# Performance work log

Measured on AMD Instinct MI355X. Metric: run time of the kernel, lower is better.

Reference implementation:

```python
import jax, jax.numpy as jnp
import numpy as np

E = 512; H = 512; L = 3; NH = 8; HD = H // NH; V = 32000
B = 64; S = 64; T = 20


def setup_inputs() -> dict:
    key = jax.random.key(0)
    ks = jax.random.split(key, 14)
    sc = 0.02
    return {
        "encoder_out": jax.random.normal(ks[0], (B, S, H), jnp.float32),
        "captions": jax.random.randint(ks[1], (B, T), 0, V),
        "embed_table": jax.random.normal(ks[2], (V, E), jnp.float32) * sc,
        "w_ih": jax.random.normal(ks[3], (L, 3 * H, E), jnp.float32) * sc,
        "w_hh": jax.random.normal(ks[4], (L, 3 * H, H), jnp.float32) * sc,
        "b_ih": jax.random.normal(ks[5], (L, 3 * H), jnp.float32) * sc,
        "b_hh": jax.random.normal(ks[6], (L, 3 * H), jnp.float32) * sc,
        "in_proj_w": jax.random.normal(ks[7], (3 * H, H), jnp.float32) * sc,
        "in_proj_b": jax.random.normal(ks[8], (3 * H,), jnp.float32) * sc,
        "out_proj_w": jax.random.normal(ks[9], (H, H), jnp.float32) * sc,
        "out_proj_b": jax.random.normal(ks[10], (H,), jnp.float32) * sc,
        "fc_w": jax.random.normal(ks[11], (V, H), jnp.float32) * sc,
        "fc_b": jax.random.normal(ks[12], (V,), jnp.float32) * sc,
    }


def _gru_cell(x, h, Wih, Whh, bih, bhh):
    # PyTorch GRUCell math. x: (B, in), h: (B, H)
    gi = x @ Wih.T + bih  # (B, 3H)
    gh = h @ Whh.T + bhh
    i_r, i_z, i_n = jnp.split(gi, 3, axis=-1)
    h_r, h_z, h_n = jnp.split(gh, 3, axis=-1)
    r = jax.nn.sigmoid(i_r + h_r)
    z = jax.nn.sigmoid(i_z + h_z)
    n = jnp.tanh(i_n + r * h_n)
    return (1.0 - z) * n + z * h


def reference(encoder_out, captions, embed_table, w_ih, w_hh, b_ih, b_hh,
              in_proj_w, in_proj_b, out_proj_w, out_proj_b, fc_w, fc_b):
    Wq, Wk, Wv = jnp.split(in_proj_w, 3, axis=0)
    bq, bk, bv = jnp.split(in_proj_b, 3, axis=0)
    # K/V projections of encoder_out are timestep-invariant: precompute once.
    Kh = (encoder_out @ Wk.T + bk).reshape(B, S, NH, HD)
    Vh = (encoder_out @ Wv.T + bv).reshape(B, S, NH, HD)
    scale = 1.0 / jnp.sqrt(jnp.float32(HD))

    emb = embed_table[captions]              # (B, T, E)
    xs = jnp.transpose(emb, (1, 0, 2))       # (T, B, E)

    def step(h, x_t):
        # h: (L, B, H); x_t: (B, E)
        new_h = []
        inp = x_t
        for l in range(L):
            hl = _gru_cell(inp, h[l], w_ih[l], w_hh[l], b_ih[l], b_hh[l])
            new_h.append(hl)
            inp = hl
        q = (inp @ Wq.T + bq).reshape(B, NH, HD)
        scores = jnp.einsum('bnd,bsnd->bns', q, Kh) * scale
        attn = jax.nn.softmax(scores, axis=-1)
        ctx = jnp.einsum('bns,bsnd->bnd', attn, Vh).reshape(B, H)
        ao = ctx @ out_proj_w.T + out_proj_b
        logits = ao @ fc_w.T + fc_b           # (B, V)
        return jnp.stack(new_h), logits

    h0 = jnp.zeros((L, B, H), dtype=encoder_out.dtype)
    _, logits = jax.lax.scan(step, h0, xs)    # logits: (T, B, V)
    return jnp.transpose(logits, (1, 0, 2))   # (B, T, V)
```

## Files before the change

kernel.cpp:

```cpp
#include <hip/hip_runtime.h>
#include <hip/hip_bf16.h>

#define TT 20
#define BB 64
#define HH 512
#define EE 512
#define VV 32000
#define NBLK 32

typedef __bf16 bf16x8 __attribute__((ext_vector_type(8)));
typedef float f32x4 __attribute__((ext_vector_type(4)));
typedef unsigned long long u64;

template <int L> struct IC { static constexpr int value = L; };

__device__ __forceinline__ void gload_lds16(const __hip_bfloat16* g, __hip_bfloat16* l) {
    __builtin_amdgcn_global_load_lds((const __attribute__((address_space(1))) void*)g,
                                     (__attribute__((address_space(3))) void*)l, 16, 0, 0);
}

__device__ __forceinline__ float sigmf(float x) { return 1.f / (1.f + __expf(-x)); }

__device__ __forceinline__ void cstore8B(void* p, u64 v) {
    __hip_atomic_store((u64*)p, v, __ATOMIC_RELAXED, __HIP_MEMORY_SCOPE_AGENT);
}
__device__ __forceinline__ void cstore4B(void* p, unsigned v) {
    __hip_atomic_store((unsigned*)p, v, __ATOMIC_RELAXED, __HIP_MEMORY_SCOPE_AGENT);
}


__global__ __launch_bounds__(256) void f2bf_kernel(const float* __restrict__ in,
                                                   __hip_bfloat16* __restrict__ out, int n) {
    int i = blockIdx.x * 256 + threadIdx.x;
    if (i < n) out[i] = __float2bfloat16(in[i]);
}

__global__ __launch_bounds__(256) void gather_emb_kernel(const float* __restrict__ tab,
                                                         const int* __restrict__ cap,
                                                         __hip_bfloat16* __restrict__ out) {
    int i = blockIdx.x * 256 + threadIdx.x;
    int e = i & (EE - 1);
    int tb = i >> 9;
    int t = tb >> 6;
    int b = tb & 63;
    int tok = cap[b * TT + t];
    out[i] = __float2bfloat16(tab[(size_t)tok * EE + e]);
}

__global__ __launch_bounds__(256) void init_kernel(__hip_bfloat16* __restrict__ hbuf,
                                                   int* __restrict__ bar) {
    int i = blockIdx.x * 256 + threadIdx.x;
    hbuf[i] = __float2bfloat16(0.f);
    if (i < 64) bar[i] = 0;
}


__global__ __launch_bounds__(256) void gemm128_kernel(
    const __hip_bfloat16* __restrict__ A,
    const __hip_bfloat16* __restrict__ Bm,
    const float* __restrict__ bias,
    float* __restrict__ C,
    __hip_bfloat16* __restrict__ Cb,
    int K, int N)
{
    __shared__ __align__(16) __hip_bfloat16 As[128 * 32];
    __shared__ __align__(16) __hip_bfloat16 Bs[128 * 32];

    int m0 = blockIdx.x * 128, n0 = blockIdx.y * 128;
    int tid = threadIdx.x;
    int wave = tid >> 6, lane = tid & 63;
    int wm = wave & 1, wn = wave >> 1;
    int row16 = lane & 15, quad = lane >> 4;

    int r0 = tid >> 2, cc = (tid & 3) * 8;
    int r1 = 64 + r0;
    const __hip_bfloat16* gA0 = A  + (size_t)(m0 + r0) * K + cc;
    const __hip_bfloat16* gA1 = A  + (size_t)(m0 + r1) * K + cc;
    const __hip_bfloat16* gB0 = Bm + (size_t)(n0 + r0) * K + cc;
    const __hip_bfloat16* gB1 = Bm + (size_t)(n0 + r1) * K + cc;
    __hip_bfloat16* lA0 = As + (size_t)(wave * 64) * 8;
    __hip_bfloat16* lA1 = As + (size_t)(256 + wave * 64) * 8;
    __hip_bfloat16* lB0 = Bs + (size_t)(wave * 64) * 8;
    __hip_bfloat16* lB1 = Bs + (size_t)(256 + wave * 64) * 8;

    const __hip_bfloat16* ra = As + (size_t)(wm * 64 + row16) * 32 + quad * 8;
    const __hip_bfloat16* rb = Bs + (size_t)(wn * 64 + row16) * 32 + quad * 8;

    f32x4 acc[4][4] = {};

    for (int k = 0; k < K; k += 32) {
        gload_lds16(gA0 + k, lA0);
        gload_lds16(gA1 + k, lA1);
        gload_lds16(gB0 + k, lB0);
        gload_lds16(gB1 + k, lB1);
        __syncthreads();
        bf16x8 af[4], bfr[4];
#pragma unroll
        for (int mt = 0; mt < 4; ++mt)
            af[mt] = *reinterpret_cast<const bf16x8*>(ra + mt * 16 * 32);
#pragma unroll
        for (int nt = 0; nt < 4; ++nt)
            bfr[nt] = *reinterpret_cast<const bf16x8*>(rb + nt * 16 * 32);
#pragma unroll
        for (int mt = 0; mt < 4; ++mt)
#pragma unroll
            for (int nt = 0; nt < 4; ++nt)
                acc[mt][nt] = __builtin_amdgcn_mfma_f32_16x16x32_bf16(af[mt], bfr[nt], acc[mt][nt], 0, 0, 0);
        __syncthreads();
    }

#pragma unroll
    for (int mt = 0; mt < 4; ++mt)
#pragma unroll
        for (int nt = 0; nt < 4; ++nt) {
            int col = n0 + wn * 64 + nt * 16 + row16;
            float bv = bias ? bias[col] : 0.f;
#pragma unroll
            for (int r = 0; r < 4; ++r) {
                int row = m0 + wm * 64 + mt * 16 + quad * 4 + r;
                size_t off = (size_t)row * N + col;
                float v = acc[mt][nt][r] + bv;
                if (Cb) Cb[off] = __float2bfloat16(v);
                else    C[off]  = v;
            }
        }
}


__global__ __launch_bounds__(512) void recurrence_kernel(
    const float* __restrict__ GI0,
    const __hip_bfloat16* __restrict__ wih,
    const __hip_bfloat16* __restrict__ whh,
    const float* __restrict__ bih,
    const float* __restrict__ bhh,
    const __hip_bfloat16* __restrict__ wq,
    const float* __restrict__ bq,
    const __hip_bfloat16* __restrict__ wo,
    const float* __restrict__ bo,
    const __hip_bfloat16* __restrict__ KVb,
    __hip_bfloat16* __restrict__ hbuf,
    float* __restrict__ qrot,
    __hip_bfloat16* __restrict__ ctxrot,
    __hip_bfloat16* __restrict__ AO,
    int* __restrict__ bar)
{
    __shared__ float smem[24 * 544];

    {
        int d = __hip_atomic_load(&bar[1], __ATOMIC_ACQUIRE, __HIP_MEMORY_SCOPE_AGENT);
        asm volatile("" :: "v"(d));
    }
    __syncthreads();

    const int tid = threadIdx.x;
    const int w = tid >> 6, lane = tid & 63;
    const int row16 = lane & 15, quad = lane >> 4;
    const int blk = blockIdx.x;
    const int c0 = blk * 16;
    const size_t HS = (size_t)64 * 512;

    f32x4 h0r = {0.f, 0.f, 0.f, 0.f}, h1r = h0r, h2r = h0r;

    int lgen = 0;
    auto gridbar = [&]() {
        asm volatile("s_waitcnt vmcnt(0)" ::: "memory");
        __syncthreads();
        if (tid == 0) {
            lgen++;
            __hip_atomic_fetch_add(&bar[0], 1, __ATOMIC_RELAXED, __HIP_MEMORY_SCOPE_AGENT);
            while (__hip_atomic_load(&bar[0], __ATOMIC_RELAXED, __HIP_MEMORY_SCOPE_AGENT) < NBLK * lgen)
                __builtin_amdgcn_s_sleep(1);
        }
        __syncthreads();
    };

#define PART(s, r, c) smem[(s) * 544 + (r) * 17 + (c)]

    auto gru_stage = [&](auto LC, int t) {
        constexpr int l = decltype(LC)::value;
        const __hip_bfloat16* hown = hbuf + ((size_t)t * 3 + l) * HS;
        const __hip_bfloat16* xin  = l ? hbuf + ((size_t)(t + 1) * 3 + (l - 1)) * HS : hown;
        const __hip_bfloat16* Wihl = wih + (size_t)l * 1536 * 512;
        const __hip_bfloat16* Whhl = whh + (size_t)l * 1536 * 512;

        int src, rh, kseg, koff;
        constexpr int nk = l ? 8 : 4;
        if (l) { src = w >> 2; rh = (w >> 1) & 1; kseg = w & 1; koff = kseg * 256; }
        else   { src = 1;      rh = w >> 2;       kseg = w & 3; koff = kseg * 128; }

        const __hip_bfloat16* Asrc = src ? hown : xin;
        const __hip_bfloat16* pa = Asrc + (size_t)(rh * 32 + row16) * 512 + koff + quad * 8;
        bf16x8 af0[nk], af1[nk];
#pragma unroll
        for (int kk = 0; kk < nk; ++kk) {
            af0[kk] = *reinterpret_cast<const bf16x8*>(pa + kk * 32);
            af1[kk] = *reinterpret_cast<const bf16x8*>(pa + (size_t)16 * 512 + kk * 32);
        }

        const __hip_bfloat16* pw = (src ? Whhl : Wihl) + (size_t)(c0 + row16) * 512 + koff + quad * 8;
        f32x4 acc[3][2] = {};
#pragma unroll
        for (int kk = 0; kk < nk; ++kk) {
            int kb = kk * 32;
#pragma unroll
            for (int g = 0; g < 3; ++g) {
                bf16x8 wv = *reinterpret_cast<const bf16x8*>(pw + (size_t)g * 262144 + kb);
                acc[g][0] = __builtin_amdgcn_mfma_f32_16x16x32_bf16(af0[kk], wv, acc[g][0], 0, 0, 0);
                acc[g][1] = __builtin_amdgcn_mfma_f32_16x16x32_bf16(af1[kk], wv, acc[g][1], 0, 0, 0);
            }
        }
#pragma unroll
        for (int g = 0; g < 3; ++g) {
            int slot = l ? (g * 8 + src * 4 + rh * 2 + kseg) : (g * 8 + rh * 4 + kseg);
#pragma unroll
            for (int mf = 0; mf < 2; ++mf)
#pragma unroll
                for (int r = 0; r < 4; ++r)
                    PART(slot, mf * 16 + quad * 4 + r, row16) = (mf ? acc[g][1][r] : acc[g][0][r]);
        }
        __syncthreads();

        if (tid < 256) {
            int row = tid >> 2, cg = tid & 3;
            int rh2 = row >> 5, lr = row & 31;
            const float* bihl = bih + l * 1536;
            const float* bhhl = bhh + l * 1536;
            f32x4& hr = (l == 0) ? h0r : (l == 1) ? h1r : h2r;
            f32x4 gi4[3];
            if (!l) {
                const float* gp = GI0 + (size_t)(t * 64 + row) * 1536 + c0 + cg * 4;
#pragma unroll
                for (int g = 0; g < 3; ++g)
                    gi4[g] = *reinterpret_cast<const f32x4*>(gp + g * 512);
            }
            union { unsigned short us[4]; u64 u; } pk;
#pragma unroll
            for (int cc = 0; cc < 4; ++cc) {
                int col16 = cg * 4 + cc, col = c0 + col16;
                float gi[3], gh[3];
#pragma unroll
                for (int g = 0; g < 3; ++g) {
                    if (l) {
                        gi[g] = PART(g * 8 + rh2 * 2, lr, col16) + PART(g * 8 + rh2 * 2 + 1, lr, col16);
                        gh[g] = PART(g * 8 + 4 + rh2 * 2, lr, col16) + PART(g * 8 + 4 + rh2 * 2 + 1, lr, col16);
                    } else {
                        gh[g] = PART(g * 8 + rh2 * 4, lr, col16) + PART(g * 8 + rh2 * 4 + 1, lr, col16) +
                                PART(g * 8 + rh2 * 4 + 2, lr, col16) + PART(g * 8 + rh2 * 4 + 3, lr, col16);
                        gi[g] = gi4[g][cc];
                    }
                }
                float rr = sigmf(gi[0] + gh[0] + bihl[col] + bhhl[col]);
                float zz = sigmf(gi[1] + gh[1] + bihl[512 + col] + bhhl[512 + col]);
                float nn = tanhf(gi[2] + bihl[1024 + col] + rr * (gh[2] + bhhl[1024 + col]));
                float hnew = (1.f - zz) * nn + zz * hr[cc];
                hr[cc] = hnew;
                __hip_bfloat16 hv = __float2bfloat16(hnew);
                pk.us[cc] = *reinterpret_cast<unsigned short*>(&hv);
            }
            cstore8B(hbuf + ((size_t)(t + 1) * 3 + l) * HS + (size_t)row * 512 + c0 + cg * 4, pk.u);
        }
        __syncthreads();
    };

    auto proj_stage = [&](const __hip_bfloat16* Asrc, const __hip_bfloat16* Wm,
                          const float* bias, bool to_q, int t) {
        int rh = w >> 2, kseg = w & 3, koff = kseg * 128;
        const __hip_bfloat16* pa = Asrc + (size_t)(rh * 32 + row16) * 512 + koff + quad * 8;
        bf16x8 af0[4], af1[4];
#pragma unroll
        for (int kk = 0; kk < 4; ++kk) {
            af0[kk] = *reinterpret_cast<const bf16x8*>(pa + kk * 32);
            af1[kk] = *reinterpret_cast<const bf16x8*>(pa + (size_t)16 * 512 + kk * 32);
        }
        const __hip_bfloat16* pw = Wm + (size_t)(c0 + row16) * 512 + koff + quad * 8;
        f32x4 a0 = {0.f, 0.f, 0.f, 0.f}, a1 = a0;
#pragma unroll
        for (int kk = 0; kk < 4; ++kk) {
            bf16x8 wv = *reinterpret_cast<const bf16x8*>(pw + kk * 32);
            a0 = __builtin_amdgcn_mfma_f32_16x16x32_bf16(af0[kk], wv, a0, 0, 0, 0);
            a1 = __builtin_amdgcn_mfma_f32_16x16x32_bf16(af1[kk], wv, a1, 0, 0, 0);
        }
#pragma unroll
        for (int r = 0; r < 4; ++r) {
            PART(w, quad * 4 + r, row16) = a0[r];
            PART(w, 16 + quad * 4 + r, row16) = a1[r];
        }
        __syncthreads();
        if (tid < 256) {
            int row = tid >> 2, cg = tid & 3;
            int rh2 = row >> 5, lr = row & 31;
            float v[4];
#pragma unroll
            for (int cc = 0; cc < 4; ++cc) {
                int col16 = cg * 4 + cc;
                float s = bias[c0 + col16];
#pragma unroll
                for (int ks = 0; ks < 4; ++ks) s += PART(rh2 * 4 + ks, lr, col16);
                v[cc] = s;
            }
            if (to_q) {
                float* dst = qrot + (size_t)t * HS + (size_t)row * 512 + c0 + cg * 4;
                union { float f[2]; u64 u; } p0, p1;
                p0.f[0] = v[0]; p0.f[1] = v[1];
                p1.f[0] = v[2]; p1.f[1] = v[3];
                cstore8B(dst, p0.u);
                cstore8B(dst + 2, p1.u);
            } else {
                union { unsigned short us[4]; u64 u; } pk;
#pragma unroll
                for (int cc = 0; cc < 4; ++cc) {
                    __hip_bfloat16 hv = __float2bfloat16(v[cc]);
                    pk.us[cc] = *reinterpret_cast<unsigned short*>(&hv);
                }
                cstore8B(AO + ((size_t)row * TT + t) * 512 + c0 + cg * 4, pk.u);
            }
        }
        __syncthreads();
    };

    auto attn_stage = [&](int t) {
        float* qls = smem;
        const float* qsrc = qrot + (size_t)t * HS;
        if (tid < 256) {
            int rr = tid >> 7, off = (tid & 127) * 4;
            f32x4 v = *reinterpret_cast<const f32x4*>(qsrc + (size_t)(blk + rr * 32) * 512 + off);
            *reinterpret_cast<f32x4*>(qls + rr * 512 + off) = v;
        }
        __syncthreads();
#pragma unroll 1
        for (int rr = 0; rr < 2; ++rr) {
            int b = blk + rr * 32;
            const float* qh = qls + rr * 512 + w * 64;
            const __hip_bfloat16* kr = KVb + (size_t)(b * 64 + lane) * 1024 + w * 64;
            float sc = 0.f;
#pragma unroll
            for (int k8 = 0; k8 < 8; ++k8) {
                bf16x8 kv = *reinterpret_cast<const bf16x8*>(kr + k8 * 8);
                const float* qv = qh + k8 * 8;
#pragma unroll
                for (int e = 0; e < 8; ++e) sc += qv[e] * (float)kv[e];
            }
            sc *= 0.125f;
            float m = sc;
            for (int off = 32; off; off >>= 1) m = fmaxf(m, __shfl_xor(m, off, 64));
            float e = __expf(sc - m);
            float s = e;
            for (int off = 32; off; off >>= 1) s += __shfl_xor(s, off, 64);
            float p = e / s;
            const __hip_bfloat16* vb = KVb + (size_t)(b * 64) * 1024 + 512 + w * 64 + lane;
            float acc = 0.f;
#pragma unroll
            for (int si = 0; si < 64; ++si)
                acc += __shfl(p, si, 64) * (float)vb[(size_t)si * 1024];
            float hi = __shfl_down(acc, 1, 64);
            if (!(lane & 1)) {
                __hip_bfloat16 e0 = __float2bfloat16(acc), e1 = __float2bfloat16(hi);
                unsigned pk = (unsigned)*reinterpret_cast<unsigned short*>(&e0) |
                              ((unsigned)*reinterpret_cast<unsigned short*>(&e1) << 16);
                cstore4B(ctxrot + (size_t)t * HS + (size_t)b * 512 + w * 64 + lane, pk);
            }
        }
        __syncthreads();
    };

#pragma unroll 1
    for (int t = 0; t < TT; ++t) {
        gru_stage(IC<0>{}, t); gridbar();
        gru_stage(IC<1>{}, t); gridbar();
        gru_stage(IC<2>{}, t); gridbar();
        proj_stage(hbuf + ((size_t)(t + 1) * 3 + 2) * HS, wq, bq, true, t); gridbar();
        attn_stage(t); gridbar();
        proj_stage(ctxrot + (size_t)t * HS, wo, bo, false, t);
    }
#undef PART
}


extern "C" void kernel_launch(void* const* d_in, const int* in_sizes, int n_in,
                              void* d_out, int out_size, void* d_ws, size_t ws_size,
                              hipStream_t stream) {
    const float* enc        = (const float*)d_in[0];
    const int*   cap        = (const int*)d_in[1];
    const float* emb_tab    = (const float*)d_in[2];
    const float* w_ih       = (const float*)d_in[3];
    const float* w_hh       = (const float*)d_in[4];
    const float* b_ih       = (const float*)d_in[5];
    const float* b_hh       = (const float*)d_in[6];
    const float* in_proj_w  = (const float*)d_in[7];
    const float* in_proj_b  = (const float*)d_in[8];
    const float* out_proj_w = (const float*)d_in[9];
    const float* out_proj_b = (const float*)d_in[10];
    const float* fc_w       = (const float*)d_in[11];
    const float* fc_b       = (const float*)d_in[12];
    float* out = (float*)d_out;

    char* p = (char*)d_ws;
    auto alloc = [&](size_t bytes) {
        char* r = p;
        p += (bytes + 255) & ~(size_t)255;
        return r;
    };
    __hip_bfloat16* fcw_bf  = (__hip_bfloat16*)alloc((size_t)VV * HH * 2);
    __hip_bfloat16* enc_bf  = (__hip_bfloat16*)alloc((size_t)BB * 64 * HH * 2);
    __hip_bfloat16* inp_bf  = (__hip_bfloat16*)alloc((size_t)1536 * 512 * 2);
    __hip_bfloat16* wih_bf  = (__hip_bfloat16*)alloc((size_t)3 * 1536 * 512 * 2);
    __hip_bfloat16* whh_bf  = (__hip_bfloat16*)alloc((size_t)3 * 1536 * 512 * 2);
    __hip_bfloat16* wo_bf   = (__hip_bfloat16*)alloc((size_t)512 * 512 * 2);
    __hip_bfloat16* xemb_bf = (__hip_bfloat16*)alloc((size_t)TT * BB * EE * 2);
    __hip_bfloat16* KVb = (__hip_bfloat16*)alloc((size_t)4096 * 1024 * 2);
    float* GI0  = (float*)alloc((size_t)1280 * 1536 * 4);
    __hip_bfloat16* hbuf = (__hip_bfloat16*)alloc((size_t)(TT + 1) * 3 * 64 * 512 * 2);
    float* qrot = (float*)alloc((size_t)TT * 64 * 512 * 4);
    __hip_bfloat16* ctxrot = (__hip_bfloat16*)alloc((size_t)TT * 64 * 512 * 2);
    __hip_bfloat16* AO = (__hip_bfloat16*)alloc((size_t)1280 * 512 * 2);
    int* bar = (int*)alloc(256);

    auto cvt = [&](const float* src, __hip_bfloat16* dst, int n) {
        f2bf_kernel<<<(n + 255) / 256, 256, 0, stream>>>(src, dst, n);
    };
    cvt(fc_w, fcw_bf, VV * HH);
    cvt(enc, enc_bf, BB * 64 * HH);
    cvt(in_proj_w, inp_bf, 1536 * 512);
    cvt(w_ih, wih_bf, 3 * 1536 * 512);
    cvt(w_hh, whh_bf, 3 * 1536 * 512);
    cvt(out_proj_w, wo_bf, 512 * 512);
    gather_emb_kernel<<<(TT * BB * EE) / 256, 256, 0, stream>>>(emb_tab, cap, xemb_bf);
    init_kernel<<<(3 * 64 * 512) / 256, 256, 0, stream>>>(hbuf, bar);

    gemm128_kernel<<<dim3(32, 8), 256, 0, stream>>>(
        enc_bf, inp_bf + 512 * 512, in_proj_b + 512, nullptr, KVb, 512, 1024);

    gemm128_kernel<<<dim3(10, 12), 256, 0, stream>>>(
        xemb_bf, wih_bf, nullptr, GI0, nullptr, 512, 1536);

    recurrence_kernel<<<NBLK, 512, 0, stream>>>(
        GI0, wih_bf, whh_bf, b_ih, b_hh,
        inp_bf, in_proj_b, wo_bf, out_proj_b,
        KVb, hbuf, qrot, ctxrot, AO, bar);

    gemm128_kernel<<<dim3(10, 250), 256, 0, stream>>>(
        AO, fcw_bf, fc_b, out, nullptr, 512, VV);
}
```

Baseline: 2.202 ms.

## Fuse Q-proj, attention and out-proj per block; replace atomic counter grid barrier with flag array

The Q projection, attention and output projection that follow the GRU layers now run inside one per-block stage. Each block owns two batch rows and computes all 512 output columns itself, so the two grid barriers and the global q/ctx round trips between those stages go away. The grid barrier itself changes from a single atomic counter to per-block generation flags, which one wavefront polls in parallel. In exchange, every block now streams the full Wq and Wo matrices with scalar FMA loops instead of MFMA, which adds redundant weight reads and compute.

Result: slower. 2.561 ms (+16.3%).

```diff
diff --git a/kernel.cpp b/kernel.cpp
--- a/kernel.cpp
+++ b/kernel.cpp
@@ -24,8 +24,8 @@
 __device__ __forceinline__ void cstore8B(void* p, u64 v) {
     __hip_atomic_store((u64*)p, v, __ATOMIC_RELAXED, __HIP_MEMORY_SCOPE_AGENT);
 }
-__device__ __forceinline__ void cstore4B(void* p, unsigned v) {
-    __hip_atomic_store((unsigned*)p, v, __ATOMIC_RELAXED, __HIP_MEMORY_SCOPE_AGENT);
+__device__ __forceinline__ void cstore4B(void* p, int v) {
+    __hip_atomic_store((int*)p, v, __ATOMIC_RELAXED, __HIP_MEMORY_SCOPE_AGENT);
 }
 
 
@@ -51,7 +51,7 @@
                                                    int* __restrict__ bar) {
     int i = blockIdx.x * 256 + threadIdx.x;
     hbuf[i] = __float2bfloat16(0.f);
-    if (i < 64) bar[i] = 0;
+    if (i < 1024) bar[i] = 0;
 }
 
 
@@ -139,15 +139,13 @@
     const float* __restrict__ bo,
     const __hip_bfloat16* __restrict__ KVb,
     __hip_bfloat16* __restrict__ hbuf,
-    float* __restrict__ qrot,
-    __hip_bfloat16* __restrict__ ctxrot,
     __hip_bfloat16* __restrict__ AO,
     int* __restrict__ bar)
 {
     __shared__ float smem[24 * 544];
 
     {
-        int d = __hip_atomic_load(&bar[1], __ATOMIC_ACQUIRE, __HIP_MEMORY_SCOPE_AGENT);
+        int d = __hip_atomic_load(&bar[1023], __ATOMIC_ACQUIRE, __HIP_MEMORY_SCOPE_AGENT);
         asm volatile("" :: "v"(d));
     }
     __syncthreads();
@@ -165,11 +163,16 @@
     auto gridbar = [&]() {
         asm volatile("s_waitcnt vmcnt(0)" ::: "memory");
         __syncthreads();
-        if (tid == 0) {
-            lgen++;
-            __hip_atomic_fetch_add(&bar[0], 1, __ATOMIC_RELAXED, __HIP_MEMORY_SCOPE_AGENT);
-            while (__hip_atomic_load(&bar[0], __ATOMIC_RELAXED, __HIP_MEMORY_SCOPE_AGENT) < NBLK * lgen)
+        lgen++;
+        if (w == 0) {
+            if (lane == 0)
+                cstore4B(&bar[blk * 16], lgen);
+            int idx = (lane & 31) * 16;
+            int v;
+            do {
                 __builtin_amdgcn_s_sleep(1);
+                v = __hip_atomic_load(&bar[idx], __ATOMIC_RELAXED, __HIP_MEMORY_SCOPE_AGENT);
+            } while (__any(v < lgen));
         }
         __syncthreads();
     };
@@ -262,76 +265,46 @@
         __syncthreads();
     };
 
-    auto proj_stage = [&](const __hip_bfloat16* Asrc, const __hip_bfloat16* Wm,
-                          const float* bias, bool to_q, int t) {
-        int rh = w >> 2, kseg = w & 3, koff = kseg * 128;
-        const __hip_bfloat16* pa = Asrc + (size_t)(rh * 32 + row16) * 512 + koff + quad * 8;
-        bf16x8 af0[4], af1[4];
-#pragma unroll
-        for (int kk = 0; kk < 4; ++kk) {
-            af0[kk] = *reinterpret_cast<const bf16x8*>(pa + kk * 32);
-            af1[kk] = *reinterpret_cast<const bf16x8*>(pa + (size_t)16 * 512 + kk * 32);
-        }
-        const __hip_bfloat16* pw = Wm + (size_t)(c0 + row16) * 512 + koff + quad * 8;
-        f32x4 a0 = {0.f, 0.f, 0.f, 0.f}, a1 = a0;
-#pragma unroll
-        for (int kk = 0; kk < 4; ++kk) {
-            bf16x8 wv = *reinterpret_cast<const bf16x8*>(pw + kk * 32);
-            a0 = __builtin_amdgcn_mfma_f32_16x16x32_bf16(af0[kk], wv, a0, 0, 0, 0);
-            a1 = __builtin_amdgcn_mfma_f32_16x16x32_bf16(af1[kk], wv, a1, 0, 0, 0);
-        }
-#pragma unroll
-        for (int r = 0; r < 4; ++r) {
-            PART(w, quad * 4 + r, row16) = a0[r];
-            PART(w, 16 + quad * 4 + r, row16) = a1[r];
-        }
-        __syncthreads();
-        if (tid < 256) {
-            int row = tid >> 2, cg = tid & 3;
-            int rh2 = row >> 5, lr = row & 31;
-            float v[4];
-#pragma unroll
-            for (int cc = 0; cc < 4; ++cc) {
-                int col16 = cg * 4 + cc;
-                float s = bias[c0 + col16];
-#pragma unroll
-                for (int ks = 0; ks < 4; ++ks) s += PART(rh2 * 4 + ks, lr, col16);
-                v[cc] = s;
-            }
-            if (to_q) {
-                float* dst = qrot + (size_t)t * HS + (size_t)row * 512 + c0 + cg * 4;
-                union { float f[2]; u64 u; } p0, p1;
-                p0.f[0] = v[0]; p0.f[1] = v[1];
-                p1.f[0] = v[2]; p1.f[1] = v[3];
-                cstore8B(dst, p0.u);
-                cstore8B(dst + 2, p1.u);
-            } else {
-                union { unsigned short us[4]; u64 u; } pk;
-#pragma unroll
-                for (int cc = 0; cc < 4; ++cc) {
-                    __hip_bfloat16 hv = __float2bfloat16(v[cc]);
-                    pk.us[cc] = *reinterpret_cast<unsigned short*>(&hv);
+    auto attn_chain = [&](int t) {
+        float* h2ls = smem;
+        float* qls  = smem + 1024;
+        float* ctxls= smem + 2048;
+        const __hip_bfloat16* h2b = hbuf + ((size_t)(t + 1) * 3 + 2) * HS;
+        const int b0 = blk * 2;
+
+        if (tid < 128) {
+            int bl = tid >> 6, k8 = tid & 63;
+            bf16x8 hv = *reinterpret_cast<const bf16x8*>(h2b + (size_t)(b0 + bl) * 512 + k8 * 8);
+            float* d = h2ls + bl * 512 + k8 * 8;
+#pragma unroll
+            for (int e = 0; e < 8; ++e) d[e] = (float)hv[e];
+        }
+        __syncthreads();
+
+        {
+            const __hip_bfloat16* wrow = wq + (size_t)tid * 512;
+            float s0 = bq[tid], s1 = s0;
+#pragma unroll 4
+            for (int k8 = 0; k8 < 64; ++k8) {
+                bf16x8 wv = *reinterpret_cast<const bf16x8*>(wrow + k8 * 8);
+#pragma unroll
+                for (int e = 0; e < 8; ++e) {
+                    float wf = (float)wv[e];
+                    s0 += h2ls[k8 * 8 + e] * wf;
+                    s1 += h2ls[512 + k8 * 8 + e] * wf;
                 }
-                cstore8B(AO + ((size_t)row * TT + t) * 512 + c0 + cg * 4, pk.u);
-            }
-        }
-        __syncthreads();
-    };
-
-    auto attn_stage = [&](int t) {
-        float* qls = smem;
-        const float* qsrc = qrot + (size_t)t * HS;
-        if (tid < 256) {
-            int rr = tid >> 7, off = (tid & 127) * 4;
-            f32x4 v = *reinterpret_cast<const f32x4*>(qsrc + (size_t)(blk + rr * 32) * 512 + off);
-            *reinterpret_cast<f32x4*>(qls + rr * 512 + off) = v;
-        }
-        __syncthreads();
+            }
+            qls[tid] = s0;
+            qls[512 + tid] = s1;
+        }
+        __syncthreads();
+
 #pragma unroll 1
-        for (int rr = 0; rr < 2; ++rr) {
-            int b = blk + rr * 32;
-            const float* qh = qls + rr * 512 + w * 64;
-            const __hip_bfloat16* kr = KVb + (size_t)(b * 64 + lane) * 1024 + w * 64;
+        for (int pp = w; pp < 16; pp += 8) {
+            int bl = pp & 1, nh = (pp >> 1) & 7;
+            int b = b0 + bl;
+            const float* qh = qls + bl * 512 + nh * 64;
+            const __hip_bfloat16* kr = KVb + (size_t)(b * 64 + lane) * 1024 + nh * 64;
             float sc = 0.f;
 #pragma unroll
             for (int k8 = 0; k8 < 8; ++k8) {
@@ -347,18 +320,30 @@
             float s = e;
             for (int off = 32; off; off >>= 1) s += __shfl_xor(s, off, 64);
             float p = e / s;
-            const __hip_bfloat16* vb = KVb + (size_t)(b * 64) * 1024 + 512 + w * 64 + lane;
+            const __hip_bfloat16* vb = KVb + (size_t)(b * 64) * 1024 + 512 + nh * 64 + lane;
             float acc = 0.f;
 #pragma unroll
             for (int si = 0; si < 64; ++si)
                 acc += __shfl(p, si, 64) * (float)vb[(size_t)si * 1024];
-            float hi = __shfl_down(acc, 1, 64);
-            if (!(lane & 1)) {
-                __hip_bfloat16 e0 = __float2bfloat16(acc), e1 = __float2bfloat16(hi);
-                unsigned pk = (unsigned)*reinterpret_cast<unsigned short*>(&e0) |
-                              ((unsigned)*reinterpret_cast<unsigned short*>(&e1) << 16);
-                cstore4B(ctxrot + (size_t)t * HS + (size_t)b * 512 + w * 64 + lane, pk);
-            }
+            ctxls[bl * 512 + nh * 64 + lane] = acc;
+        }
+        __syncthreads();
+
+        {
+            const __hip_bfloat16* wrow = wo + (size_t)tid * 512;
+            float s0 = bo[tid], s1 = s0;
+#pragma unroll 4
+            for (int k8 = 0; k8 < 64; ++k8) {
+                bf16x8 wv = *reinterpret_cast<const bf16x8*>(wrow + k8 * 8);
+#pragma unroll
+                for (int e = 0; e < 8; ++e) {
+                    float wf = (float)wv[e];
+                    s0 += ctxls[k8 * 8 + e] * wf;
+                    s1 += ctxls[512 + k8 * 8 + e] * wf;
+                }
+            }
+            AO[((size_t)b0 * TT + t) * 512 + tid] = __float2bfloat16(s0);
+            AO[((size_t)(b0 + 1) * TT + t) * 512 + tid] = __float2bfloat16(s1);
         }
         __syncthreads();
     };
@@ -368,9 +353,7 @@
         gru_stage(IC<0>{}, t); gridbar();
         gru_stage(IC<1>{}, t); gridbar();
         gru_stage(IC<2>{}, t); gridbar();
-        proj_stage(hbuf + ((size_t)(t + 1) * 3 + 2) * HS, wq, bq, true, t); gridbar();
-        attn_stage(t); gridbar();
-        proj_stage(ctxrot + (size_t)t * HS, wo, bo, false, t);
+        attn_chain(t);
     }
 #undef PART
 }
@@ -410,10 +393,8 @@
     __hip_bfloat16* KVb = (__hip_bfloat16*)alloc((size_t)4096 * 1024 * 2);
     float* GI0  = (float*)alloc((size_t)1280 * 1536 * 4);
     __hip_bfloat16* hbuf = (__hip_bfloat16*)alloc((size_t)(TT + 1) * 3 * 64 * 512 * 2);
-    float* qrot = (float*)alloc((size_t)TT * 64 * 512 * 4);
-    __hip_bfloat16* ctxrot = (__hip_bfloat16*)alloc((size_t)TT * 64 * 512 * 2);
     __hip_bfloat16* AO = (__hip_bfloat16*)alloc((size_t)1280 * 512 * 2);
-    int* bar = (int*)alloc(256);
+    int* bar = (int*)alloc(4096);
 
     auto cvt = [&](const float* src, __hip_bfloat16* dst, int n) {
         f2bf_kernel<<<(n + 255) / 256, 256, 0, stream>>>(src, dst, n);
@@ -436,7 +417,7 @@
     recurrence_kernel<<<NBLK, 512, 0, stream>>>(
         GI0, wih_bf, whh_bf, b_ih, b_hh,
         inp_bf, in_proj_b, wo_bf, out_proj_b,
-        KVb, hbuf, qrot, ctxrot, AO, bar);
+        KVb, hbuf, AO, bar);
 
     gemm128_kernel<<<dim3(10, 250), 256, 0, stream>>>(
         AO, fcw_bf, fc_b, out, nullptr, 512, VV);
```
